# Performance work log

Hardware: AMD Instinct MI355X
Metric: run time of the kernel (lower is better)

Reference implementation:

```python
import jax, jax.numpy as jnp
import numpy as np

N_NODES = 50000
N_EDGES = 800000
IN_F = 256
HEADS = 4
C = 32  # out_features // heads = 128 // 4
OUT_F = HEADS * C
NEG_SLOPE = 0.2
BN_EPS = 1e-5


def setup_inputs() -> dict:
    key = jax.random.key(0)
    ks = jax.random.split(key, 6)
    x = jax.random.normal(ks[0], (N_NODES, IN_F), dtype=jnp.float32)
    edge_index = jax.random.randint(ks[1], (2, N_EDGES), 0, N_NODES, dtype=jnp.int64)
    W = jax.random.normal(ks[2], (IN_F, OUT_F), dtype=jnp.float32) * 0.05
    att_src = jax.random.normal(ks[3], (HEADS, C), dtype=jnp.float32) * 0.05
    att_dst = jax.random.normal(ks[4], (HEADS, C), dtype=jnp.float32) * 0.05
    bias = jnp.zeros((OUT_F,), dtype=jnp.float32)
    gamma = jnp.ones((OUT_F,), dtype=jnp.float32)
    beta = jnp.zeros((OUT_F,), dtype=jnp.float32)
    return {"x": x, "edge_index": edge_index, "W": W, "att_src": att_src,
            "att_dst": att_dst, "bias": bias, "gamma": gamma, "beta": beta}


def reference(x, edge_index, W, att_src, att_dst, bias, gamma, beta):
    N = x.shape[0]
    # PyG GATConv adds self-loops by default
    loops = jnp.arange(N, dtype=edge_index.dtype)
    src = jnp.concatenate([edge_index[0], loops])  # [E+N]
    dst = jnp.concatenate([edge_index[1], loops])  # [E+N]

    h = (x @ W).reshape(N, HEADS, C)               # [N, H, C]
    a_src = jnp.sum(h * att_src, axis=-1)          # [N, H]
    a_dst = jnp.sum(h * att_dst, axis=-1)          # [N, H]

    e = a_src[src] + a_dst[dst]                    # [E', H]
    e = jax.nn.leaky_relu(e, NEG_SLOPE)
    # segment softmax over destination neighborhoods (self-loops ensure no empty segments)
    e_max = jax.ops.segment_max(e, dst, num_segments=N)
    e = jnp.exp(e - e_max[dst])
    denom = jax.ops.segment_sum(e, dst, num_segments=N)
    alpha = e / (denom[dst] + 1e-16)               # [E', H]

    msg = h[src] * alpha[:, :, None]               # [E', H, C]
    out = jax.ops.segment_sum(msg, dst, num_segments=N).reshape(N, OUT_F) + bias

    # BatchNorm1d in training mode (batch statistics, biased variance)
    mean = jnp.mean(out, axis=0)
    var = jnp.var(out, axis=0)
    out = (out - mean) * jax.lax.rsqrt(var + BN_EPS) * gamma + beta
    # ELU; dropout is identity in eval / deterministic reference
    return jax.nn.elu(out)
```

## Files before the change

### kernel.cpp

```cpp
#include <hip/hip_runtime.h>
#include <hip/hip_fp16.h>
#include <math.h>

#define NN 50000
#define EE 800000
#define EP (EE + NN)
#define INF_ 256
#define OF 128
#define NEG_SLOPE 0.2f
#define BN_EPS 1e-5f
#define NB 196
#define NWIN 8
#define DPW 6250
#define NCH 32
#define QPC 6250

typedef _Float16 half8 __attribute__((ext_vector_type(8)));
typedef float floatx4 __attribute__((ext_vector_type(4)));
typedef int intx4 __attribute__((ext_vector_type(4)));

__device__ __forceinline__ float lrelu_exp(float v) {
    v = v > 0.f ? v : NEG_SLOPE * v;
    return expf(v);
}

__global__ __launch_bounds__(256) void k_wprep(const float* __restrict__ W, _Float16* __restrict__ wfrag,
                                               float* __restrict__ fsum)
{
    int idx = blockIdx.x * 256 + threadIdx.x;
    if (idx < 256) fsum[idx] = 0.f;
    int j   = idx & 7;
    int l   = (idx >> 3) & 63;
    int t   = (idx >> 9) & 7;
    int ksg = idx >> 12;
    int k   = ksg * 32 + ((l >> 4) << 3) + j;
    int col = t * 16 + (l & 15);
    wfrag[idx] = (_Float16)W[k * OF + col];
}

__global__ __launch_bounds__(256) void k_gemm(
    const float* __restrict__ x, const _Float16* __restrict__ wfrag,
    const float* __restrict__ att_s, const float* __restrict__ att_d,
    _Float16* __restrict__ h, float* __restrict__ a_src, float* __restrict__ a_dst)
{
    __shared__ __align__(16) _Float16 smem[8192];
    _Float16* xh = smem;

    const int tid  = threadIdx.x;
    const int l    = tid & 63;
    const int w    = tid >> 6;
    const int row0 = blockIdx.x * 64;
    const int lrow = l & 15;
    const int lk8  = (l >> 4) << 3;

    floatx4 acc[8];
    #pragma unroll
    for (int t = 0; t < 8; ++t) acc[t] = (floatx4){0.f, 0.f, 0.f, 0.f};

    for (int kc = 0; kc < 4; ++kc) {
        __syncthreads();
        #pragma unroll
        for (int it = 0; it < 4; ++it) {
            int i  = tid + (it << 8);
            int r  = i >> 4;
            int c4 = (i & 15) << 2;
            int rr = row0 + r; if (rr >= NN) rr = NN - 1;
            float4 v = *(const float4*)&x[rr * INF_ + (kc << 6) + c4];
            _Float16* p = &xh[r * 72 + c4];
            p[0] = (_Float16)v.x; p[1] = (_Float16)v.y;
            p[2] = (_Float16)v.z; p[3] = (_Float16)v.w;
        }
        __syncthreads();
        #pragma unroll
        for (int ks = 0; ks < 2; ++ks) {
            int ksg = kc * 2 + ks;
            half8 a = *(half8*)&xh[(w * 16 + lrow) * 72 + (ks << 5) + lk8];
            const _Float16* wf = &wfrag[(ksg << 12) + (l << 3)];
            #pragma unroll
            for (int t = 0; t < 8; ++t) {
                half8 b = *(const half8*)&wf[t << 9];
                acc[t] = __builtin_amdgcn_mfma_f32_16x16x32_f16(a, b, acc[t], 0, 0, 0);
            }
        }
    }

    float as_c[8], ad_c[8];
    #pragma unroll
    for (int t = 0; t < 8; ++t) { as_c[t] = att_s[t * 16 + lrow]; ad_c[t] = att_d[t * 16 + lrow]; }
    float my_s = 0.f, my_d = 0.f;
    #pragma unroll
    for (int hh = 0; hh < 4; ++hh) {
        #pragma unroll
        for (int reg = 0; reg < 4; ++reg) {
            float ps = acc[2*hh][reg] * as_c[2*hh] + acc[2*hh+1][reg] * as_c[2*hh+1];
            float pd = acc[2*hh][reg] * ad_c[2*hh] + acc[2*hh+1][reg] * ad_c[2*hh+1];
            ps += __shfl_xor(ps, 1); ps += __shfl_xor(ps, 2); ps += __shfl_xor(ps, 4); ps += __shfl_xor(ps, 8);
            pd += __shfl_xor(pd, 1); pd += __shfl_xor(pd, 2); pd += __shfl_xor(pd, 4); pd += __shfl_xor(pd, 8);
            if (lrow == hh * 4 + reg) { my_s = ps; my_d = pd; }
        }
    }
    {
        int myreg = lrow & 3, myhh = lrow >> 2;
        int myrow = row0 + w * 16 + ((l >> 4) << 2) + myreg;
        if (myrow < NN) { a_src[myrow * 4 + myhh] = my_s; a_dst[myrow * 4 + myhh] = my_d; }
    }

    __syncthreads();
    _Float16* ldso = smem + w * 2048;
    #pragma unroll
    for (int t = 0; t < 8; ++t)
        #pragma unroll
        for (int reg = 0; reg < 4; ++reg)
            ldso[(((l >> 4) << 2) + reg) * 128 + t * 16 + lrow] = (_Float16)acc[t][reg];
    __syncthreads();
    {
        _Float16* gdst = h + (size_t)(row0 + w * 16) * OF;
        #pragma unroll
        for (int q = 0; q < 4; ++q) {
            int off = (q << 9) + (l << 3);
            *(half8*)&gdst[off] = *(half8*)&ldso[off];
        }
    }
}

__global__ __launch_bounds__(1024) void k_winhist(const int* __restrict__ ei, int* __restrict__ counts2)
{
    __shared__ int hist[DPW];
    const int w   = blockIdx.x & 7;
    const int c   = blockIdx.x >> 3;
    const int dlo = w * DPW;
    for (int i = threadIdx.x; i < DPW; i += 1024) hist[i] = 0;
    __syncthreads();
    const int q0 = c * QPC;
    for (int q = q0 + threadIdx.x; q < q0 + QPC; q += 1024) {
        intx4 d4 = __builtin_nontemporal_load(((const intx4*)(ei + EE)) + q);
        int dj[4] = {d4.x, d4.y, d4.z, d4.w};
        #pragma unroll
        for (int j = 0; j < 4; ++j) {
            unsigned d = (unsigned)(dj[j] - dlo);
            if (d < DPW) atomicAdd(&hist[d], 1);
        }
    }
    __syncthreads();
    int* dst = counts2 + c * NN + dlo;
    for (int i = threadIdx.x; i < DPW; i += 1024) dst[i] = hist[i];
}

__global__ __launch_bounds__(256) void k_blocksum(const int* __restrict__ counts2, int* __restrict__ partials)
{
    int i = blockIdx.x * 256 + threadIdx.x;
    int v = 0;
    if (i < NN) {
        v = 1;
        #pragma unroll 8
        for (int c = 0; c < NCH; ++c) v += counts2[c * NN + i];
    }
    v += __shfl_xor(v, 1);  v += __shfl_xor(v, 2);  v += __shfl_xor(v, 4);
    v += __shfl_xor(v, 8);  v += __shfl_xor(v, 16); v += __shfl_xor(v, 32);
    __shared__ int wsum[4];
    if ((threadIdx.x & 63) == 0) wsum[threadIdx.x >> 6] = v;
    __syncthreads();
    if (threadIdx.x == 0) partials[blockIdx.x] = wsum[0] + wsum[1] + wsum[2] + wsum[3];
}

__global__ __launch_bounds__(256) void k_writerows(
    const int* __restrict__ counts2, const int* __restrict__ partials,
    int* __restrict__ row_start, int* __restrict__ csr_src, int* __restrict__ base)
{
    __shared__ int smp[256];
    __shared__ int sm[256];
    int t = threadIdx.x;

    int pv = (t < NB) ? partials[t] : 0;
    smp[t] = pv;
    __syncthreads();
    for (int off = 1; off < 256; off <<= 1) {
        int u = (t >= off) ? smp[t - off] : 0;
        __syncthreads();
        smp[t] += u;
        __syncthreads();
    }
    int blockoff = (blockIdx.x > 0) ? smp[blockIdx.x - 1] : 0;

    int i = blockIdx.x * 256 + t;
    int v = 0;
    if (i < NN) {
        v = 1;
        #pragma unroll 8
        for (int c = 0; c < NCH; ++c) v += counts2[c * NN + i];
    }
    sm[t] = v;
    __syncthreads();
    for (int off = 1; off < 256; off <<= 1) {
        int u = (t >= off) ? sm[t - off] : 0;
        __syncthreads();
        sm[t] += u;
        __syncthreads();
    }
    int excl = blockoff + sm[t] - v;
    if (i < NN) {
        row_start[i] = excl;
        csr_src[excl] = i;
        int p = excl + 1;
        #pragma unroll 8
        for (int c = 0; c < NCH; ++c) { base[c * NN + i] = p; p += counts2[c * NN + i]; }
    }
    if (i == NN) row_start[NN] = excl;
}

__global__ __launch_bounds__(1024) void k_winfill(
    const int* __restrict__ ei, const int* __restrict__ base, int* __restrict__ csr_src)
{
    __shared__ int pos[DPW];
    const int w   = blockIdx.x & 7;
    const int c   = blockIdx.x >> 3;
    const int dlo = w * DPW;
    for (int i = threadIdx.x; i < DPW; i += 1024) pos[i] = base[c * NN + dlo + i];
    __syncthreads();
    const int q0 = c * QPC;
    for (int q = q0 + threadIdx.x; q < q0 + QPC; q += 1024) {
        intx4 d4 = __builtin_nontemporal_load(((const intx4*)(ei + EE)) + q);
        int idx0 = q << 2;
        int dj[4] = {d4.x, d4.y, d4.z, d4.w};
        #pragma unroll
        for (int j = 0; j < 4; ++j) {
            unsigned d = (unsigned)(dj[j] - dlo);
            if (d < DPW) {
                int p = atomicAdd(&pos[d], 1);
                csr_src[p] = ei[idx0 + j];
            }
        }
    }
}

__global__ __launch_bounds__(256) void k_gather(
    const _Float16* __restrict__ h, const int* __restrict__ csr_src,
    const int* __restrict__ row_start, const float* __restrict__ a_src,
    const float* __restrict__ a_dst, const float* __restrict__ bias,
    _Float16* __restrict__ outh)
{
    int node = blockIdx.x * 4 + (threadIdx.x >> 6);
    int lane = threadIdx.x & 63;
    int g    = lane >> 4;
    int c    = lane & 15;
    int head = c >> 2;
    int b = row_start[node];
    int e = row_start[node + 1];
    float ad = a_dst[(node << 2) + head];

    float acc[8] = {};
    float dsum = 0.f;
    for (int k = b; k < e; k += 4) {
        int  kk  = k + g;
        bool act = kk < e;
        int  kc  = act ? kk : b;
        int  s   = csr_src[kc];
        float a  = lrelu_exp(a_src[(s << 2) + head] + ad);
        if (!act) a = 0.f;
        dsum += a;
        half8 hv = *(const half8*)&h[(size_t)s * OF + (c << 3)];
        #pragma unroll
        for (int j = 0; j < 8; ++j)
            acc[j] = fmaf(a, (float)hv[j], acc[j]);
    }
    #pragma unroll
    for (int j = 0; j < 8; ++j) {
        acc[j] += __shfl_xor(acc[j], 16);
        acc[j] += __shfl_xor(acc[j], 32);
    }
    dsum += __shfl_xor(dsum, 16);
    dsum += __shfl_xor(dsum, 32);
    if (g == 0) {
        float inv = 1.0f / (dsum + 1e-16f);
        float4 b0 = *(const float4*)&bias[c << 3];
        float4 b1 = *(const float4*)&bias[(c << 3) + 4];
        float bj[8] = {b0.x, b0.y, b0.z, b0.w, b1.x, b1.y, b1.z, b1.w};
        half8 o;
        #pragma unroll
        for (int j = 0; j < 8; ++j)
            o[j] = (_Float16)fmaf(acc[j], inv, bj[j]);
        *(half8*)&outh[(size_t)node * OF + (c << 3)] = o;
    }
}

__global__ __launch_bounds__(256) void k_bnred(
    const _Float16* __restrict__ outh, float* __restrict__ fsum, float* __restrict__ fsumsq)
{
    int f = threadIdx.x & 127;
    int r = blockIdx.x * 2 + (threadIdx.x >> 7);
    float s = 0.f, ss = 0.f;
    for (; r < NN; r += gridDim.x * 2) {
        float v = (float)outh[r * OF + f];
        s += v;
        ss = fmaf(v, v, ss);
    }
    atomicAdd(&fsum[f], s);
    atomicAdd(&fsumsq[f], ss);
}

__global__ __launch_bounds__(256) void k_apply(
    const _Float16* __restrict__ outh, const float* __restrict__ fsum,
    const float* __restrict__ fsumsq, const float* __restrict__ gamma,
    const float* __restrict__ beta, float* __restrict__ out)
{
    __shared__ float ssc[128], ssh[128];
    if (threadIdx.x < 128) {
        int f = threadIdx.x;
        float mean = fsum[f] * (1.0f / NN);
        float var  = fsumsq[f] * (1.0f / NN) - mean * mean;
        float sc   = gamma[f] * rsqrtf(var + BN_EPS);
        ssc[f] = sc;
        ssh[f] = beta[f] - mean * sc;
    }
    __syncthreads();
    int i    = blockIdx.x * 256 + threadIdx.x;
    int base = i << 3;
    int f    = base & 127;
    half8 v  = *(const half8*)&outh[base];
    float r[8];
    #pragma unroll
    for (int j = 0; j < 8; ++j) {
        float t = fmaf((float)v[j], ssc[f + j], ssh[f + j]);
        r[j] = t > 0.f ? t : expm1f(t);
    }
    *(float4*)&out[base]     = make_float4(r[0], r[1], r[2], r[3]);
    *(float4*)&out[base + 4] = make_float4(r[4], r[5], r[6], r[7]);
}

extern "C" void kernel_launch(void* const* d_in, const int* in_sizes, int n_in,
                              void* d_out, int out_size, void* d_ws, size_t ws_size,
                              hipStream_t stream)
{
    const float* x     = (const float*)d_in[0];
    const int*   ei    = (const int*)d_in[1];
    const float* W     = (const float*)d_in[2];
    const float* att_s = (const float*)d_in[3];
    const float* att_d = (const float*)d_in[4];
    const float* bias  = (const float*)d_in[5];
    const float* gamma = (const float*)d_in[6];
    const float* beta  = (const float*)d_in[7];
    float* out = (float*)d_out;

    float* ws           = (float*)d_ws;
    _Float16* h         = (_Float16*)ws;
    _Float16* outh      = (_Float16*)(ws + 3210000);
    float* a_src        = ws + 6410000;
    float* a_dst        = a_src + 200000;
    float* wfrag_f      = a_dst + 200000;
    float* scratch_f    = wfrag_f + 20000;
    float* fsum         = scratch_f + 1700000;
    float* fsumsq       = fsum + 128;
    int* row_start      = (int*)(fsumsq + 128);
    int* csr_src        = row_start + NN + 1;
    int* partials       = csr_src + EP;
    int* counts2        = (int*)scratch_f;
    int* cbase          = (int*)outh;
    _Float16* wfrag     = (_Float16*)wfrag_f;

    k_wprep<<<128, 256, 0, stream>>>(W, wfrag, fsum);
    k_gemm<<<(NN + 63) / 64, 256, 0, stream>>>(x, wfrag, att_s, att_d, h, a_src, a_dst);
    k_winhist<<<NWIN * NCH, 1024, 0, stream>>>(ei, counts2);
    k_blocksum<<<NB, 256, 0, stream>>>(counts2, partials);
    k_writerows<<<NB, 256, 0, stream>>>(counts2, partials, row_start, csr_src, cbase);
    k_winfill<<<NWIN * NCH, 1024, 0, stream>>>(ei, cbase, csr_src);
    k_gather<<<NN / 4, 256, 0, stream>>>(h, csr_src, row_start, a_src, a_dst, bias, outh);
    k_bnred<<<512, 256, 0, stream>>>(outh, fsum, fsumsq);
    k_apply<<<NN * OF / 8 / 256, 256, 0, stream>>>(outh, fsum, fsumsq, gamma, beta, out);
}
```

Before: 155.8 us.

## Store h head-major and split gather work per head across blocks

The GEMM now writes h in a head-major layout, one [HPAD x 32] fp16 plane per head. The gather kernel is relaunched with four blocks per node group, one per head, and each wavefront handles 8 edges at a time with 64-byte rows per head. The aim is a smaller per-head gather working set (3.2 MB instead of 12.8 MB) for better L2/MALL locality on random neighbor reads, and more parallelism per node. The trade-off is that csr_src, row_start and a_src are now read four times, the loads are narrower half4, and there is an extra shuffle-reduction level. The h buffer must hold 4*HPAD*32 elements, and HPAD padding has to be covered by the existing allocation.

```diff
diff --git a/kernel.cpp b/kernel.cpp
--- a/kernel.cpp
+++ b/kernel.cpp
@@ -7,6 +7,7 @@
 #define EP (EE + NN)
 #define INF_ 256
 #define OF 128
+#define HPAD 50048
 #define NEG_SLOPE 0.2f
 #define BN_EPS 1e-5f
 #define NB 196
@@ -16,6 +17,7 @@
 #define QPC 6250
 
 typedef _Float16 half8 __attribute__((ext_vector_type(8)));
+typedef _Float16 half4 __attribute__((ext_vector_type(4)));
 typedef float floatx4 __attribute__((ext_vector_type(4)));
 typedef int intx4 __attribute__((ext_vector_type(4)));
 
@@ -114,11 +116,15 @@
             ldso[(((l >> 4) << 2) + reg) * 128 + t * 16 + lrow] = (_Float16)acc[t][reg];
     __syncthreads();
     {
-        _Float16* gdst = h + (size_t)(row0 + w * 16) * OF;
+        int rowbase = row0 + w * 16;
         #pragma unroll
         for (int q = 0; q < 4; ++q) {
             int off = (q << 9) + (l << 3);
-            *(half8*)&gdst[off] = *(half8*)&ldso[off];
+            int r   = off >> 7;
+            int col = off & 127;
+            int hh  = col >> 5;
+            int ch  = col & 31;
+            *(half8*)&h[(size_t)hh * (HPAD * 32) + (size_t)(rowbase + r) * 32 + ch] = *(half8*)&ldso[off];
         }
     }
 }
@@ -239,18 +245,19 @@
     const float* __restrict__ a_dst, const float* __restrict__ bias,
     _Float16* __restrict__ outh)
 {
-    int node = blockIdx.x * 4 + (threadIdx.x >> 6);
+    int head = blockIdx.x & 3;
+    int node = (blockIdx.x >> 2) * 4 + (threadIdx.x >> 6);
     int lane = threadIdx.x & 63;
-    int g    = lane >> 4;
-    int c    = lane & 15;
-    int head = c >> 2;
+    int g    = lane >> 3;
+    int c    = lane & 7;
     int b = row_start[node];
     int e = row_start[node + 1];
     float ad = a_dst[(node << 2) + head];
-
-    float acc[8] = {};
+    const _Float16* hs = h + (size_t)head * (HPAD * 32);
+
+    float acc[4] = {};
     float dsum = 0.f;
-    for (int k = b; k < e; k += 4) {
+    for (int k = b; k < e; k += 8) {
         int  kk  = k + g;
         bool act = kk < e;
         int  kc  = act ? kk : b;
@@ -258,28 +265,30 @@
         float a  = lrelu_exp(a_src[(s << 2) + head] + ad);
         if (!act) a = 0.f;
         dsum += a;
-        half8 hv = *(const half8*)&h[(size_t)s * OF + (c << 3)];
-        #pragma unroll
-        for (int j = 0; j < 8; ++j)
+        half4 hv = *(const half4*)&hs[(size_t)s * 32 + (c << 2)];
+        #pragma unroll
+        for (int j = 0; j < 4; ++j)
             acc[j] = fmaf(a, (float)hv[j], acc[j]);
     }
     #pragma unroll
-    for (int j = 0; j < 8; ++j) {
+    for (int j = 0; j < 4; ++j) {
+        acc[j] += __shfl_xor(acc[j], 8);
         acc[j] += __shfl_xor(acc[j], 16);
         acc[j] += __shfl_xor(acc[j], 32);
     }
+    dsum += __shfl_xor(dsum, 8);
     dsum += __shfl_xor(dsum, 16);
     dsum += __shfl_xor(dsum, 32);
     if (g == 0) {
         float inv = 1.0f / (dsum + 1e-16f);
-        float4 b0 = *(const float4*)&bias[c << 3];
-        float4 b1 = *(const float4*)&bias[(c << 3) + 4];
-        float bj[8] = {b0.x, b0.y, b0.z, b0.w, b1.x, b1.y, b1.z, b1.w};
-        half8 o;
-        #pragma unroll
-        for (int j = 0; j < 8; ++j)
-            o[j] = (_Float16)fmaf(acc[j], inv, bj[j]);
-        *(half8*)&outh[(size_t)node * OF + (c << 3)] = o;
+        int col = head * 32 + (c << 2);
+        float4 bj = *(const float4*)&bias[col];
+        float bb[4] = {bj.x, bj.y, bj.z, bj.w};
+        half4 o;
+        #pragma unroll
+        for (int j = 0; j < 4; ++j)
+            o[j] = (_Float16)fmaf(acc[j], inv, bb[j]);
+        *(half4*)&outh[(size_t)node * OF + col] = o;
     }
 }
 
@@ -363,7 +372,7 @@
     k_blocksum<<<NB, 256, 0, stream>>>(counts2, partials);
     k_writerows<<<NB, 256, 0, stream>>>(counts2, partials, row_start, csr_src, cbase);
     k_winfill<<<NWIN * NCH, 1024, 0, stream>>>(ei, cbase, csr_src);
-    k_gather<<<NN / 4, 256, 0, stream>>>(h, csr_src, row_start, a_src, a_dst, bias, outh);
+    k_gather<<<(NN / 4) * 4, 256, 0, stream>>>(h, csr_src, row_start, a_src, a_dst, bias, outh);
     k_bnred<<<512, 256, 0, stream>>>(outh, fsum, fsumsq);
     k_apply<<<NN * OF / 8 / 256, 256, 0, stream>>>(outh, fsum, fsumsq, gamma, beta, out);
 }
```

After: 198.6 us. 27.5% more time.
